# Optimization experiments

Hardware: AMD Instinct MI355X
Metric: run time of the kernel (lower is better)

Reference implementation:

```python
import jax, jax.numpy as jnp
import numpy as np

N_HEADS = 16
N_KV_HEADS = 4
HEAD_DIM = 128


def apply_rope(x, cos, sin):
    # x: [b, h, s, head_dim]; cos/sin: [1, 1, s, head_dim//2]
    d = x.shape[-1] // 2
    x1, x2 = x[..., :d], x[..., d:]
    return jnp.concatenate([x1 * cos - x2 * sin, x1 * sin + x2 * cos], axis=-1)


def setup_inputs() -> dict:
    key = jax.random.key(0)
    ks = jax.random.split(key, 9)
    b, s, dim = 2, 2048, 2048
    inp = {
        "x": jax.random.normal(ks[0], (b, s, dim), jnp.float32),
        "cos": jax.random.normal(ks[1], (1, 1, s, HEAD_DIM // 2), jnp.float32),
        "sin": jax.random.normal(ks[2], (1, 1, s, HEAD_DIM // 2), jnp.float32),
        "Wq": jax.random.normal(ks[3], (dim, N_HEADS * HEAD_DIM), jnp.float32) * 0.02,
        "bq": jax.random.normal(ks[4], (N_HEADS * HEAD_DIM,), jnp.float32) * 0.02,
        "Wkv": jax.random.normal(ks[5], (dim, 2 * N_KV_HEADS * HEAD_DIM), jnp.float32) * 0.02,
        "bkv": jax.random.normal(ks[6], (2 * N_KV_HEADS * HEAD_DIM,), jnp.float32) * 0.02,
        "Wo": jax.random.normal(ks[7], (N_HEADS * HEAD_DIM, dim), jnp.float32) * 0.02,
        "bo": jax.random.normal(ks[8], (dim,), jnp.float32) * 0.02,
        "causal": 1,
    }
    return inp


def reference(x, cos, sin, Wq, bq, Wkv, bkv, Wo, bo, causal):
    b, s, dim = x.shape
    scale = 1.0 / np.sqrt(HEAD_DIM)
    # QKV projections (torch Linear with weight stored transposed here)
    q = (x @ Wq + bq).reshape(b, s, N_HEADS, HEAD_DIM).transpose(0, 2, 1, 3)
    kv = x @ Wkv + bkv  # [b, s, 2*n_kv*hd]
    k, v = jnp.split(kv, 2, axis=-1)
    k = k.reshape(b, s, N_KV_HEADS, HEAD_DIM).transpose(0, 2, 1, 3)
    v = v.reshape(b, s, N_KV_HEADS, HEAD_DIM).transpose(0, 2, 1, 3)
    q = apply_rope(q, cos, sin)
    k = apply_rope(k, cos, sin)
    # GQA: repeat kv heads
    rep = N_HEADS // N_KV_HEADS
    k = jnp.repeat(k, rep, axis=1)
    v = jnp.repeat(v, rep, axis=1)
    logits = jnp.einsum("bhqd,bhkd->bhqk", q, k) * scale
    if causal:
        mask = jnp.tril(jnp.ones((s, s), dtype=bool))
        logits = jnp.where(mask[None, None], logits, jnp.finfo(logits.dtype).min)
    scores = jax.nn.softmax(logits, axis=-1)
    vo = jnp.einsum("bhqk,bhkd->bhqd", scores, v)
    vo = vo.transpose(0, 2, 1, 3).reshape(b, s, N_HEADS * HEAD_DIM)
    out = vo @ Wo + bo
    return out
```

## Files before the change

### kernel.cpp

```cpp
#include <hip/hip_runtime.h>
#include <hip/hip_bf16.h>

typedef __bf16 bf16x8 __attribute__((ext_vector_type(8)));
typedef float  f32x4  __attribute__((ext_vector_type(4)));
typedef unsigned int u32;

#define GLD_LDS16(gp, lp) __builtin_amdgcn_global_load_lds( \
    (const __attribute__((address_space(1))) u32*)(gp), \
    (__attribute__((address_space(3))) u32*)(lp), 16, 0, 0)

template<int CTRL>
__device__ __forceinline__ float dpp_rot(float x) {
    int y = __builtin_amdgcn_update_dpp(__float_as_int(x), __float_as_int(x),
                                        CTRL, 0xF, 0xF, false);
    return __int_as_float(y);
}
__device__ __forceinline__ float rowmax16(float x) {
    x = fmaxf(x, dpp_rot<0x121>(x));
    x = fmaxf(x, dpp_rot<0x122>(x));
    x = fmaxf(x, dpp_rot<0x124>(x));
    x = fmaxf(x, dpp_rot<0x128>(x));
    return x;
}
__device__ __forceinline__ float rowsum16(float x) {
    x += dpp_rot<0x121>(x);
    x += dpp_rot<0x122>(x);
    x += dpp_rot<0x124>(x);
    x += dpp_rot<0x128>(x);
    return x;
}


__global__ __launch_bounds__(256) void f32_to_bf16_kernel(
    const float* __restrict__ in, __bf16* __restrict__ out, size_t n) {
    size_t i = ((size_t)blockIdx.x * 256 + threadIdx.x) * 8;
    if (i >= n) return;
    float4 a = *(const float4*)(in + i);
    float4 b = *(const float4*)(in + i + 4);
    bf16x8 v;
    v[0] = (__bf16)a.x; v[1] = (__bf16)a.y; v[2] = (__bf16)a.z; v[3] = (__bf16)a.w;
    v[4] = (__bf16)b.x; v[5] = (__bf16)b.y; v[6] = (__bf16)b.z; v[7] = (__bf16)b.w;
    *(bf16x8*)(out + i) = v;
}

__global__ __launch_bounds__(256) void transpose_to_bf16_kernel(
    const float* __restrict__ W, __bf16* __restrict__ Wt, int K, int N) {
    __shared__ float tile[32][33];
    int n0 = blockIdx.x * 32, k0 = blockIdx.y * 32;
    int tx = threadIdx.x, ty = threadIdx.y;
    #pragma unroll
    for (int i = 0; i < 32; i += 8)
        tile[ty + i][tx] = W[(size_t)(k0 + ty + i) * N + n0 + tx];
    __syncthreads();
    #pragma unroll
    for (int i = 0; i < 32; i += 8)
        Wt[(size_t)(n0 + ty + i) * K + k0 + tx] = (__bf16)tile[tx][ty + i];
}

__global__ __launch_bounds__(256) void concat_bias_kernel(
    const float* __restrict__ bq, const float* __restrict__ bkv,
    float* __restrict__ bqkv) {
    int i = blockIdx.x * 256 + threadIdx.x;
    if (i < 2048) bqkv[i] = bq[i];
    else if (i < 3072) bqkv[i] = bkv[i - 2048];
}

__global__ __launch_bounds__(256) void transpose_v_kernel(
    const __bf16* __restrict__ qkv, __bf16* __restrict__ vtg, int S) {
    __shared__ __bf16 tile[32][33];
    int s0 = blockIdx.x * 32, d0 = blockIdx.y * 32, z = blockIdx.z;
    int b = z >> 2, kvh = z & 3;
    int tx = threadIdx.x, ty = threadIdx.y;
    #pragma unroll
    for (int i = 0; i < 32; i += 8)
        tile[ty + i][tx] =
            qkv[((size_t)b * S + s0 + ty + i) * 3072 + 2560 + kvh * 128 + d0 + tx];
    __syncthreads();
    #pragma unroll
    for (int i = 0; i < 32; i += 8)
        vtg[((size_t)z * 128 + d0 + ty + i) * S + s0 + tx] = tile[tx][ty + i];
}

#define BM 128
#define BN 128
#define BK 64

template <typename OutT>
__global__ __launch_bounds__(256) void gemm_bt_bias_kernel(
    const __bf16* __restrict__ A, const __bf16* __restrict__ Bt,
    const float* __restrict__ bias, OutT* __restrict__ C,
    int M, int N, int K) {
    __shared__ __bf16 As[BM * BK];
    __shared__ __bf16 Bs[BN * BK];
    int tid  = threadIdx.x;
    int bm   = blockIdx.x;
    int bn   = blockIdx.y;
    int wave = tid >> 6;
    int lane = tid & 63;
    int wm   = (wave >> 1) * 64;
    int wn   = (wave & 1) * 64;
    int quad = lane >> 4;
    int l16  = lane & 15;
    int gr   = wave * 32 + (lane >> 3);
    int gc   = (lane & 7) * 8;

    f32x4 acc[4][4];
    f32x4 zero = {0.f, 0.f, 0.f, 0.f};
    #pragma unroll
    for (int i = 0; i < 4; ++i)
        #pragma unroll
        for (int j = 0; j < 4; ++j) acc[i][j] = zero;

    const __bf16* Abase = A  + (size_t)(bm * BM) * K;
    const __bf16* Bbase = Bt + (size_t)(bn * BN) * K;

    for (int k0 = 0; k0 < K; k0 += BK) {
        if (k0) __syncthreads();
        #pragma unroll
        for (int i = 0; i < 4; ++i) {
            GLD_LDS16(Abase + (size_t)(gr + i * 8) * K + k0 + gc,
                      &As[(wave * 32 + i * 8) * BK]);
            GLD_LDS16(Bbase + (size_t)(gr + i * 8) * K + k0 + gc,
                      &Bs[(wave * 32 + i * 8) * BK]);
        }
        __syncthreads();

        bf16x8 af[4][2], bf[4][2];
        #pragma unroll
        for (int i = 0; i < 4; ++i)
            #pragma unroll
            for (int kc = 0; kc < 2; ++kc)
                af[i][kc] = *(bf16x8*)&As[(wm + i * 16 + l16) * BK + kc * 32 + quad * 8];
        #pragma unroll
        for (int j = 0; j < 4; ++j)
            #pragma unroll
            for (int kc = 0; kc < 2; ++kc)
                bf[j][kc] = *(bf16x8*)&Bs[(wn + j * 16 + l16) * BK + kc * 32 + quad * 8];
        #pragma unroll
        for (int kc = 0; kc < 2; ++kc)
            #pragma unroll
            for (int i = 0; i < 4; ++i)
                #pragma unroll
                for (int j = 0; j < 4; ++j)
                    acc[i][j] = __builtin_amdgcn_mfma_f32_16x16x32_bf16(
                        af[i][kc], bf[j][kc], acc[i][j], 0, 0, 0);
    }

    #pragma unroll
    for (int i = 0; i < 4; ++i) {
        int row = bm * BM + wm + i * 16 + quad * 4;
        #pragma unroll
        for (int j = 0; j < 4; ++j) {
            int col  = bn * BN + wn + j * 16 + l16;
            float bv = bias[col];
            #pragma unroll
            for (int r = 0; r < 4; ++r)
                C[(size_t)(row + r) * N + col] = (OutT)(acc[i][j][r] + bv);
        }
    }
}

__global__ __launch_bounds__(256) void rope_kernel(
    __bf16* __restrict__ buf, const float* __restrict__ cosp,
    const float* __restrict__ sinp, int heads, int rowstride, int coloff,
    int S, int total) {
    int idx = blockIdx.x * 256 + threadIdx.x;
    if (idx >= total) return;
    int d  = idx & 63;
    int t2 = idx >> 6;
    int h  = t2 % heads;
    int r  = t2 / heads;
    int s  = r & (S - 1);
    size_t base = (size_t)r * rowstride + coloff + h * 128;
    float x1 = (float)buf[base + d];
    float x2 = (float)buf[base + d + 64];
    float c  = cosp[s * 64 + d];
    float sn = sinp[s * 64 + d];
    buf[base + d]      = (__bf16)(x1 * c - x2 * sn);
    buf[base + d + 64] = (__bf16)(x1 * sn + x2 * c);
}


__global__ __launch_bounds__(256) void flash_mfma_kernel(
    const __bf16* __restrict__ qkv,
    const __bf16* __restrict__ vtg,
    __bf16* __restrict__ vo,
    const int* __restrict__ causal_p, int S) {
    __shared__ __bf16 Ks[2][64 * 128];
    __shared__ __bf16 Ps[4 * 16 * 64];

    const int QKV = 3072;
    int tid  = threadIdx.x;
    int wave = tid >> 6;
    int lane = tid & 63;
    int quad = lane >> 4;
    int l16  = lane & 15;
    int id   = blockIdx.x;
    int xcd  = id & 7;
    int b    = xcd >> 2;
    int kvh  = xcd & 3;
    int rest = id >> 3;
    int hh   = rest & 3;
    int qti  = rest >> 2;
    int qt   = 31 - qti;
    int h    = kvh * 4 + hh;
    int causal = causal_p[0];
    const float SCALE = 0.08838834764831845f;

    const __bf16* vB = vtg + ((size_t)(b * 4 + kvh) * 128) * S;
    char* psw = (char*)Ps + wave * 2048;

    int q0 = qt * 64;
    int nt = causal ? (qt + 1) : (S / 64);

    bf16x8 a_frag[4];
    size_t qrow = ((size_t)b * S + q0 + wave * 16 + l16) * QKV + h * 128 + quad * 8;
    #pragma unroll
    for (int kc = 0; kc < 4; ++kc)
        a_frag[kc] = *(const bf16x8*)(qkv + qrow + kc * 32);

    f32x4 o_acc[8];
    f32x4 zero4 = {0.f, 0.f, 0.f, 0.f};
    #pragma unroll
    for (int dt = 0; dt < 8; ++dt) o_acc[dt] = zero4;
    float m_[4], l_[4];
    #pragma unroll
    for (int r = 0; r < 4; ++r) { m_[r] = -1e30f; l_[r] = 0.f; }
    int qrow_d = q0 + wave * 16 + quad * 4;

    {
        size_t kg = ((size_t)b * S + wave * 16 + l16) * QKV + 2048 + kvh * 128 + quad * 8;
        #pragma unroll
        for (int kc = 0; kc < 4; ++kc)
            GLD_LDS16(qkv + kg + kc * 32, &Ks[0][(wave * 4 + kc) * 512]);
    }

    for (int t = 0; t < nt; ++t) {
        int cur = t & 1;
        __syncthreads();
        if (t + 1 < nt) {
            size_t kg = ((size_t)b * S + (t + 1) * 64 + wave * 16 + l16) * QKV
                        + 2048 + kvh * 128 + quad * 8;
            #pragma unroll
            for (int kc = 0; kc < 4; ++kc)
                GLD_LDS16(qkv + kg + kc * 32, &Ks[1 - cur][(wave * 4 + kc) * 512]);
        }
        int j0 = t * 64;

        bf16x8 vf[8][2];
        #pragma unroll
        for (int dt = 0; dt < 8; ++dt) {
            const __bf16* vp = vB + (size_t)(dt * 16 + l16) * S + j0 + quad * 8;
            vf[dt][0] = *(const bf16x8*)(vp);
            vf[dt][1] = *(const bf16x8*)(vp + 32);
        }

        f32x4 s_t[4];
        #pragma unroll
        for (int jt = 0; jt < 4; ++jt) s_t[jt] = zero4;
        #pragma unroll
        for (int jt = 0; jt < 4; ++jt)
            #pragma unroll
            for (int kc = 0; kc < 4; ++kc) {
                bf16x8 kf = *(bf16x8*)&Ks[cur][(jt * 4 + kc) * 512 + lane * 8];
                s_t[jt] = __builtin_amdgcn_mfma_f32_16x16x32_bf16(
                    a_frag[kc], kf, s_t[jt], 0, 0, 0);
            }

        int diag = causal && (t == nt - 1);
        #pragma unroll
        for (int jt = 0; jt < 4; ++jt)
            #pragma unroll
            for (int r = 0; r < 4; ++r) {
                float sv = s_t[jt][r] * SCALE;
                if (diag && (j0 + jt * 16 + l16 > qrow_d + r)) sv = -1e30f;
                s_t[jt][r] = sv;
            }

        float alpha[4];
        #pragma unroll
        for (int r = 0; r < 4; ++r) {
            float v = fmaxf(fmaxf(s_t[0][r], s_t[1][r]),
                            fmaxf(s_t[2][r], s_t[3][r]));
            v = rowmax16(v);
            float m_new = fmaxf(m_[r], v);
            alpha[r] = __expf(m_[r] - m_new);
            m_[r] = m_new;
            float rs = 0.f;
            #pragma unroll
            for (int jt = 0; jt < 4; ++jt) {
                float p = __expf(s_t[jt][r] - m_new);
                s_t[jt][r] = p;
                rs += p;
            }
            l_[r] = l_[r] * alpha[r] + rs;
        }
        #pragma unroll
        for (int jt = 0; jt < 4; ++jt)
            #pragma unroll
            for (int r = 0; r < 4; ++r) {
                int prow = quad * 4 + r;
                int inb  = (jt * 16 + l16) * 2;
                *(__bf16*)(psw + prow * 128 + (inb ^ ((prow & 7) << 4))) =
                    (__bf16)s_t[jt][r];
            }
        #pragma unroll
        for (int dt = 0; dt < 8; ++dt)
            #pragma unroll
            for (int r = 0; r < 4; ++r) o_acc[dt][r] *= alpha[r];

        int rb  = l16 * 128;
        int swz = (l16 & 7) << 4;
        bf16x8 p0 = *(bf16x8*)(psw + rb + ((quad * 16) ^ swz));
        bf16x8 p1 = *(bf16x8*)(psw + rb + ((64 + quad * 16) ^ swz));
        #pragma unroll
        for (int dt = 0; dt < 8; ++dt) {
            o_acc[dt] = __builtin_amdgcn_mfma_f32_16x16x32_bf16(
                p0, vf[dt][0], o_acc[dt], 0, 0, 0);
            o_acc[dt] = __builtin_amdgcn_mfma_f32_16x16x32_bf16(
                p1, vf[dt][1], o_acc[dt], 0, 0, 0);
        }
    }

    float invl[4];
    #pragma unroll
    for (int r = 0; r < 4; ++r) invl[r] = 1.f / rowsum16(l_[r]);
    size_t obase = ((size_t)b * S + q0 + wave * 16 + quad * 4) * 2048
                   + h * 128 + l16;
    #pragma unroll
    for (int dt = 0; dt < 8; ++dt)
        #pragma unroll
        for (int r = 0; r < 4; ++r)
            vo[obase + (size_t)r * 2048 + dt * 16] = (__bf16)(o_acc[dt][r] * invl[r]);
}


extern "C" void kernel_launch(void* const* d_in, const int* in_sizes, int n_in,
                              void* d_out, int out_size, void* d_ws, size_t ws_size,
                              hipStream_t stream) {
    const float* x    = (const float*)d_in[0];
    const float* cosp = (const float*)d_in[1];
    const float* sinp = (const float*)d_in[2];
    const float* Wq   = (const float*)d_in[3];
    const float* bq   = (const float*)d_in[4];
    const float* Wkv  = (const float*)d_in[5];
    const float* bkv  = (const float*)d_in[6];
    const float* Wo   = (const float*)d_in[7];
    const float* bo   = (const float*)d_in[8];
    const int* causal = (const int*)d_in[9];
    float* out = (float*)d_out;

    const int B = 2, S = 2048;
    const int M = B * S;

    char* w = (char*)d_ws;
    __bf16* x16    = (__bf16*)w; w += (size_t)M * 2048 * 2;
    __bf16* Wqkvt  = (__bf16*)w; w += (size_t)3072 * 2048 * 2;
    __bf16* Wot    = (__bf16*)w; w += (size_t)2048 * 2048 * 2;
    float*  bqkv   = (float*)w;  w += (size_t)3072 * 4;
    __bf16* qkvbuf = (__bf16*)w; w += (size_t)M * 3072 * 2;
    __bf16* vobuf  = x16;
    __bf16* vtg    = Wqkvt;

    f32_to_bf16_kernel<<<(M * 2048) / (256 * 8), 256, 0, stream>>>(x, x16, (size_t)M * 2048);
    transpose_to_bf16_kernel<<<dim3(2048 / 32, 2048 / 32), dim3(32, 8), 0, stream>>>(Wq, Wqkvt, 2048, 2048);
    transpose_to_bf16_kernel<<<dim3(1024 / 32, 2048 / 32), dim3(32, 8), 0, stream>>>(Wkv, Wqkvt + (size_t)2048 * 2048, 2048, 1024);
    transpose_to_bf16_kernel<<<dim3(2048 / 32, 2048 / 32), dim3(32, 8), 0, stream>>>(Wo, Wot, 2048, 2048);
    concat_bias_kernel<<<12, 256, 0, stream>>>(bq, bkv, bqkv);
    gemm_bt_bias_kernel<__bf16><<<dim3(M / BM, 3072 / BN), 256, 0, stream>>>(x16, Wqkvt, bqkv, qkvbuf, M, 3072, 2048);
    {
        int totq = M * 16 * 64;
        rope_kernel<<<(totq + 255) / 256, 256, 0, stream>>>(qkvbuf, cosp, sinp, 16, 3072, 0, S, totq);
        int totk = M * 4 * 64;
        rope_kernel<<<(totk + 255) / 256, 256, 0, stream>>>(qkvbuf, cosp, sinp, 4, 3072, 2048, S, totk);
    }
    transpose_v_kernel<<<dim3(S / 32, 128 / 32, B * 4), dim3(32, 8), 0, stream>>>(qkvbuf, vtg, S);
    flash_mfma_kernel<<<dim3(1024), 256, 0, stream>>>(qkvbuf, vtg, vobuf, causal, S);
    gemm_bt_bias_kernel<float><<<dim3(M / BM, 2048 / BN), 256, 0, stream>>>(vobuf, Wot, bo, out, M, 2048, 2048);
}
```

Baseline: 443.4 us.

## Pair causal query tiles per block, stage V in LDS, XCD-swizzle GEMM grid

The flash kernel now gives each block two query tiles (qt and 31-qt), so causal work is balanced across 512 blocks instead of 1024 uneven ones. V tiles are double-buffered into LDS with async global-to-LDS loads alongside K, replacing direct per-lane global loads. The GEMMs switch to a 1D grid with an XCD-aware block remap so neighbouring tiles share L2. The extra 32KB of LDS for V may reduce occupancy, and running the two phases back to back serialises work within each block.

```diff
diff --git a/kernel.cpp b/kernel.cpp
--- a/kernel.cpp
+++ b/kernel.cpp
@@ -93,8 +93,12 @@
     __shared__ __bf16 As[BM * BK];
     __shared__ __bf16 Bs[BN * BK];
     int tid  = threadIdx.x;
-    int bm   = blockIdx.x;
-    int bn   = blockIdx.y;
+    int nwg  = gridDim.x;
+    int cpx  = nwg >> 3;
+    int swzb = (blockIdx.x & 7) * cpx + (blockIdx.x >> 3);
+    int nbm  = M / BM;
+    int bm   = swzb % nbm;
+    int bn   = swzb / nbm;
     int wave = tid >> 6;
     int lane = tid & 63;
     int wm   = (wave >> 1) * 64;
@@ -187,6 +191,7 @@
     __bf16* __restrict__ vo,
     const int* __restrict__ causal_p, int S) {
     __shared__ __bf16 Ks[2][64 * 128];
+    __shared__ __bf16 Vs[2][64 * 128];
     __shared__ __bf16 Ps[4 * 16 * 64];
 
     const int QKV = 3072;
@@ -201,8 +206,7 @@
     int kvh  = xcd & 3;
     int rest = id >> 3;
     int hh   = rest & 3;
-    int qti  = rest >> 2;
-    int qt   = 31 - qti;
+    int pair = rest >> 2;
     int h    = kvh * 4 + hh;
     int causal = causal_p[0];
     const float SCALE = 0.08838834764831845f;
@@ -210,128 +214,142 @@
     const __bf16* vB = vtg + ((size_t)(b * 4 + kvh) * 128) * S;
     char* psw = (char*)Ps + wave * 2048;
 
-    int q0 = qt * 64;
-    int nt = causal ? (qt + 1) : (S / 64);
-
-    bf16x8 a_frag[4];
-    size_t qrow = ((size_t)b * S + q0 + wave * 16 + l16) * QKV + h * 128 + quad * 8;
-    #pragma unroll
-    for (int kc = 0; kc < 4; ++kc)
-        a_frag[kc] = *(const bf16x8*)(qkv + qrow + kc * 32);
-
-    f32x4 o_acc[8];
-    f32x4 zero4 = {0.f, 0.f, 0.f, 0.f};
-    #pragma unroll
-    for (int dt = 0; dt < 8; ++dt) o_acc[dt] = zero4;
-    float m_[4], l_[4];
-    #pragma unroll
-    for (int r = 0; r < 4; ++r) { m_[r] = -1e30f; l_[r] = 0.f; }
-    int qrow_d = q0 + wave * 16 + quad * 4;
-
-    {
-        size_t kg = ((size_t)b * S + wave * 16 + l16) * QKV + 2048 + kvh * 128 + quad * 8;
+    #pragma unroll 1
+    for (int phase = 0; phase < 2; ++phase) {
+        int qt = phase ? (31 - pair) : pair;
+        int q0 = qt * 64;
+        int nt = causal ? (qt + 1) : (S / 64);
+
+        bf16x8 a_frag[4];
+        size_t qrow = ((size_t)b * S + q0 + wave * 16 + l16) * QKV + h * 128 + quad * 8;
         #pragma unroll
         for (int kc = 0; kc < 4; ++kc)
-            GLD_LDS16(qkv + kg + kc * 32, &Ks[0][(wave * 4 + kc) * 512]);
+            a_frag[kc] = *(const bf16x8*)(qkv + qrow + kc * 32);
+
+        f32x4 o_acc[8];
+        f32x4 zero4 = {0.f, 0.f, 0.f, 0.f};
+        #pragma unroll
+        for (int dt = 0; dt < 8; ++dt) o_acc[dt] = zero4;
+        float m_[4], l_[4];
+        #pragma unroll
+        for (int r = 0; r < 4; ++r) { m_[r] = -1e30f; l_[r] = 0.f; }
+        int qrow_d = q0 + wave * 16 + quad * 4;
+
+        __syncthreads();
+        {
+            size_t kg = ((size_t)b * S + wave * 16 + l16) * QKV + 2048 + kvh * 128 + quad * 8;
+            #pragma unroll
+            for (int kc = 0; kc < 4; ++kc)
+                GLD_LDS16(qkv + kg + kc * 32, &Ks[0][(wave * 4 + kc) * 512]);
+            #pragma unroll
+            for (int i = 0; i < 4; ++i) {
+                int c  = wave * 4 + i;
+                int dt = c >> 1, kc = c & 1;
+                GLD_LDS16(vB + (size_t)(dt * 16 + l16) * S + kc * 32 + quad * 8,
+                          &Vs[0][c * 512]);
+            }
+        }
+
+        for (int t = 0; t < nt; ++t) {
+            int cur = t & 1;
+            __syncthreads();
+            if (t + 1 < nt) {
+                size_t kg = ((size_t)b * S + (t + 1) * 64 + wave * 16 + l16) * QKV
+                            + 2048 + kvh * 128 + quad * 8;
+                #pragma unroll
+                for (int kc = 0; kc < 4; ++kc)
+                    GLD_LDS16(qkv + kg + kc * 32, &Ks[1 - cur][(wave * 4 + kc) * 512]);
+                size_t vgoff = (size_t)(t + 1) * 64;
+                #pragma unroll
+                for (int i = 0; i < 4; ++i) {
+                    int c  = wave * 4 + i;
+                    int dt = c >> 1, kc = c & 1;
+                    GLD_LDS16(vB + (size_t)(dt * 16 + l16) * S + vgoff + kc * 32 + quad * 8,
+                              &Vs[1 - cur][c * 512]);
+                }
+            }
+            int j0 = t * 64;
+
+            f32x4 s_t[4];
+            #pragma unroll
+            for (int jt = 0; jt < 4; ++jt) s_t[jt] = zero4;
+            #pragma unroll
+            for (int jt = 0; jt < 4; ++jt)
+                #pragma unroll
+                for (int kc = 0; kc < 4; ++kc) {
+                    bf16x8 kf = *(bf16x8*)&Ks[cur][(jt * 4 + kc) * 512 + lane * 8];
+                    s_t[jt] = __builtin_amdgcn_mfma_f32_16x16x32_bf16(
+                        a_frag[kc], kf, s_t[jt], 0, 0, 0);
+                }
+
+            int diag = causal && (t == nt - 1);
+            #pragma unroll
+            for (int jt = 0; jt < 4; ++jt)
+                #pragma unroll
+                for (int r = 0; r < 4; ++r) {
+                    float sv = s_t[jt][r] * SCALE;
+                    if (diag && (j0 + jt * 16 + l16 > qrow_d + r)) sv = -1e30f;
+                    s_t[jt][r] = sv;
+                }
+
+            float alpha[4];
+            #pragma unroll
+            for (int r = 0; r < 4; ++r) {
+                float v = fmaxf(fmaxf(s_t[0][r], s_t[1][r]),
+                                fmaxf(s_t[2][r], s_t[3][r]));
+                v = rowmax16(v);
+                float m_new = fmaxf(m_[r], v);
+                alpha[r] = __expf(m_[r] - m_new);
+                m_[r] = m_new;
+                float rs = 0.f;
+                #pragma unroll
+                for (int jt = 0; jt < 4; ++jt) {
+                    float p = __expf(s_t[jt][r] - m_new);
+                    s_t[jt][r] = p;
+                    rs += p;
+                }
+                l_[r] = l_[r] * alpha[r] + rs;
+            }
+            #pragma unroll
+            for (int jt = 0; jt < 4; ++jt)
+                #pragma unroll
+                for (int r = 0; r < 4; ++r) {
+                    int prow = quad * 4 + r;
+                    int inb  = (jt * 16 + l16) * 2;
+                    *(__bf16*)(psw + prow * 128 + (inb ^ ((prow & 7) << 4))) =
+                        (__bf16)s_t[jt][r];
+                }
+            #pragma unroll
+            for (int dt = 0; dt < 8; ++dt)
+                #pragma unroll
+                for (int r = 0; r < 4; ++r) o_acc[dt][r] *= alpha[r];
+
+            int rb  = l16 * 128;
+            int swz = (l16 & 7) << 4;
+            bf16x8 p0 = *(bf16x8*)(psw + rb + ((quad * 16) ^ swz));
+            bf16x8 p1 = *(bf16x8*)(psw + rb + ((64 + quad * 16) ^ swz));
+            #pragma unroll
+            for (int dt = 0; dt < 8; ++dt) {
+                bf16x8 vf0 = *(bf16x8*)&Vs[cur][(dt * 2 + 0) * 512 + lane * 8];
+                bf16x8 vf1 = *(bf16x8*)&Vs[cur][(dt * 2 + 1) * 512 + lane * 8];
+                o_acc[dt] = __builtin_amdgcn_mfma_f32_16x16x32_bf16(
+                    p0, vf0, o_acc[dt], 0, 0, 0);
+                o_acc[dt] = __builtin_amdgcn_mfma_f32_16x16x32_bf16(
+                    p1, vf1, o_acc[dt], 0, 0, 0);
+            }
+        }
+
+        float invl[4];
+        #pragma unroll
+        for (int r = 0; r < 4; ++r) invl[r] = 1.f / rowsum16(l_[r]);
+        size_t obase = ((size_t)b * S + q0 + wave * 16 + quad * 4) * 2048
+                       + h * 128 + l16;
+        #pragma unroll
+        for (int dt = 0; dt < 8; ++dt)
+            #pragma unroll
+            for (int r = 0; r < 4; ++r)
+                vo[obase + (size_t)r * 2048 + dt * 16] = (__bf16)(o_acc[dt][r] * invl[r]);
     }
-
-    for (int t = 0; t < nt; ++t) {
-        int cur = t & 1;
-        __syncthreads();
-        if (t + 1 < nt) {
-            size_t kg = ((size_t)b * S + (t + 1) * 64 + wave * 16 + l16) * QKV
-                        + 2048 + kvh * 128 + quad * 8;
-            #pragma unroll
-            for (int kc = 0; kc < 4; ++kc)
-                GLD_LDS16(qkv + kg + kc * 32, &Ks[1 - cur][(wave * 4 + kc) * 512]);
-        }
-        int j0 = t * 64;
-
-        bf16x8 vf[8][2];
-        #pragma unroll
-        for (int dt = 0; dt < 8; ++dt) {
-            const __bf16* vp = vB + (size_t)(dt * 16 + l16) * S + j0 + quad * 8;
-            vf[dt][0] = *(const bf16x8*)(vp);
-            vf[dt][1] = *(const bf16x8*)(vp + 32);
-        }
-
-        f32x4 s_t[4];
-        #pragma unroll
-        for (int jt = 0; jt < 4; ++jt) s_t[jt] = zero4;
-        #pragma unroll
-        for (int jt = 0; jt < 4; ++jt)
-            #pragma unroll
-            for (int kc = 0; kc < 4; ++kc) {
-                bf16x8 kf = *(bf16x8*)&Ks[cur][(jt * 4 + kc) * 512 + lane * 8];
-                s_t[jt] = __builtin_amdgcn_mfma_f32_16x16x32_bf16(
-                    a_frag[kc], kf, s_t[jt], 0, 0, 0);
-            }
-
-        int diag = causal && (t == nt - 1);
-        #pragma unroll
-        for (int jt = 0; jt < 4; ++jt)
-            #pragma unroll
-            for (int r = 0; r < 4; ++r) {
-                float sv = s_t[jt][r] * SCALE;
-                if (diag && (j0 + jt * 16 + l16 > qrow_d + r)) sv = -1e30f;
-                s_t[jt][r] = sv;
-            }
-
-        float alpha[4];
-        #pragma unroll
-        for (int r = 0; r < 4; ++r) {
-            float v = fmaxf(fmaxf(s_t[0][r], s_t[1][r]),
-                            fmaxf(s_t[2][r], s_t[3][r]));
-            v = rowmax16(v);
-            float m_new = fmaxf(m_[r], v);
-            alpha[r] = __expf(m_[r] - m_new);
-            m_[r] = m_new;
-            float rs = 0.f;
-            #pragma unroll
-            for (int jt = 0; jt < 4; ++jt) {
-                float p = __expf(s_t[jt][r] - m_new);
-                s_t[jt][r] = p;
-                rs += p;
-            }
-            l_[r] = l_[r] * alpha[r] + rs;
-        }
-        #pragma unroll
-        for (int jt = 0; jt < 4; ++jt)
-            #pragma unroll
-            for (int r = 0; r < 4; ++r) {
-                int prow = quad * 4 + r;
-                int inb  = (jt * 16 + l16) * 2;
-                *(__bf16*)(psw + prow * 128 + (inb ^ ((prow & 7) << 4))) =
-                    (__bf16)s_t[jt][r];
-            }
-        #pragma unroll
-        for (int dt = 0; dt < 8; ++dt)
-            #pragma unroll
-            for (int r = 0; r < 4; ++r) o_acc[dt][r] *= alpha[r];
-
-        int rb  = l16 * 128;
-        int swz = (l16 & 7) << 4;
-        bf16x8 p0 = *(bf16x8*)(psw + rb + ((quad * 16) ^ swz));
-        bf16x8 p1 = *(bf16x8*)(psw + rb + ((64 + quad * 16) ^ swz));
-        #pragma unroll
-        for (int dt = 0; dt < 8; ++dt) {
-            o_acc[dt] = __builtin_amdgcn_mfma_f32_16x16x32_bf16(
-                p0, vf[dt][0], o_acc[dt], 0, 0, 0);
-            o_acc[dt] = __builtin_amdgcn_mfma_f32_16x16x32_bf16(
-                p1, vf[dt][1], o_acc[dt], 0, 0, 0);
-        }
-    }
-
-    float invl[4];
-    #pragma unroll
-    for (int r = 0; r < 4; ++r) invl[r] = 1.f / rowsum16(l_[r]);
-    size_t obase = ((size_t)b * S + q0 + wave * 16 + quad * 4) * 2048
-                   + h * 128 + l16;
-    #pragma unroll
-    for (int dt = 0; dt < 8; ++dt)
-        #pragma unroll
-        for (int r = 0; r < 4; ++r)
-            vo[obase + (size_t)r * 2048 + dt * 16] = (__bf16)(o_acc[dt][r] * invl[r]);
 }
 
 
@@ -367,7 +385,7 @@
     transpose_to_bf16_kernel<<<dim3(1024 / 32, 2048 / 32), dim3(32, 8), 0, stream>>>(Wkv, Wqkvt + (size_t)2048 * 2048, 2048, 1024);
     transpose_to_bf16_kernel<<<dim3(2048 / 32, 2048 / 32), dim3(32, 8), 0, stream>>>(Wo, Wot, 2048, 2048);
     concat_bias_kernel<<<12, 256, 0, stream>>>(bq, bkv, bqkv);
-    gemm_bt_bias_kernel<__bf16><<<dim3(M / BM, 3072 / BN), 256, 0, stream>>>(x16, Wqkvt, bqkv, qkvbuf, M, 3072, 2048);
+    gemm_bt_bias_kernel<__bf16><<<dim3((M / BM) * (3072 / BN)), 256, 0, stream>>>(x16, Wqkvt, bqkv, qkvbuf, M, 3072, 2048);
     {
         int totq = M * 16 * 64;
         rope_kernel<<<(totq + 255) / 256, 256, 0, stream>>>(qkvbuf, cosp, sinp, 16, 3072, 0, S, totq);
@@ -375,6 +393,6 @@
         rope_kernel<<<(totk + 255) / 256, 256, 0, stream>>>(qkvbuf, cosp, sinp, 4, 3072, 2048, S, totk);
     }
     transpose_v_kernel<<<dim3(S / 32, 128 / 32, B * 4), dim3(32, 8), 0, stream>>>(qkvbuf, vtg, S);
-    flash_mfma_kernel<<<dim3(1024), 256, 0, stream>>>(qkvbuf, vtg, vobuf, causal, S);
-    gemm_bt_bias_kernel<float><<<dim3(M / BM, 2048 / BN), 256, 0, stream>>>(vobuf, Wot, bo, out, M, 2048, 2048);
-}
+    flash_mfma_kernel<<<dim3(512), 256, 0, stream>>>(qkvbuf, vtg, vobuf, causal, S);
+    gemm_bt_bias_kernel<float><<<dim3((M / BM) * (2048 / BN)), 256, 0, stream>>>(vobuf, Wot, bo, out, M, 2048, 2048);
+}
```

Measured after the change: 393.2 us. -11.3%, faster.
